# Kernel tuning notes

Measured on AMD Instinct MI355X. Metric: run time of the kernel, lower is better.

## Reference

```python
import jax, jax.numpy as jnp
import numpy as np

H = 2048      # hidden_size
I = 768       # moe_intermediate_size
E = 32        # num_experts
K = 8         # num_experts_per_tok (top_k)
T = 1024      # tokens (batch * seq)


def setup_inputs() -> dict:
    key = jax.random.key(0)
    k1, k2, k3, k4 = jax.random.split(key, 4)
    return {
        "hidden_states": jax.random.normal(k1, (T, H), jnp.float32),
        "gate_weight": jax.random.normal(k2, (E, H), jnp.float32) * 0.02,
        "w13_weight": jax.random.normal(k3, (E, 2 * I, H), jnp.float32) * 0.02,
        "w2_weight": jax.random.normal(k4, (E, H, I), jnp.float32) * 0.02,
    }


def reference(hidden_states, gate_weight, w13_weight, w2_weight):
    x = hidden_states  # [T, H]
    # --- router (Qwen3MoeSparseMoeBlock gating) ---
    logits = x @ gate_weight.T                      # [T, E]
    probs = jax.nn.softmax(logits, axis=-1)
    topk_w, topk_idx = jax.lax.top_k(probs, K)      # [T, K]
    topk_w = topk_w / jnp.sum(topk_w, axis=-1, keepdims=True)  # norm_topk_prob
    # dense combine matrix [T, E]: routing weight per (token, expert), 0 if not selected
    combine = jnp.zeros((x.shape[0], E), x.dtype).at[
        jnp.arange(x.shape[0])[:, None], topk_idx
    ].add(topk_w)
    # --- expert FFNs (fused gate+up = w13, SiLU-gated, then w2 down-proj) ---
    h = jnp.einsum('th,eoh->eto', x, w13_weight)    # [E, T, 2I]
    gate, up = h[:, :, :I], h[:, :, I:]
    act = jax.nn.silu(gate) * up                    # [E, T, I]
    y = jnp.einsum('eti,ehi->eth', act, w2_weight)  # [E, T, H]
    # --- weighted combine ---
    return jnp.einsum('eth,te->th', y, combine)     # [T, H]
```

## Files before the change

### kernel.cpp

```cpp
#include <hip/hip_runtime.h>
#include <hip/hip_bf16.h>
#include <math.h>

#define T_TOK 1024
#define H_DIM 2048
#define I_DIM 768
#define E_NUM 32
#define K_TOP 8
#define BK 32
#define GRID_P 1024

typedef __bf16 bf16x8 __attribute__((ext_vector_type(8)));
typedef float  f32x4  __attribute__((ext_vector_type(4)));

__device__ __forceinline__ bf16x8 cvt2_bf16(const f32x4 a, const f32x4 b) {
    bf16x8 r;
    r[0] = (__bf16)a[0]; r[1] = (__bf16)a[1]; r[2] = (__bf16)a[2]; r[3] = (__bf16)a[3];
    r[4] = (__bf16)b[0]; r[5] = (__bf16)b[1]; r[6] = (__bf16)b[2]; r[7] = (__bf16)b[3];
    return r;
}

__device__ __forceinline__ int frag_off(int r, int kgrp8) {
    return (r >> 4) * 512 + kgrp8 * 128 + (r & 15) * 8;
}

__global__ __launch_bounds__(256) void cvtx_kernel(
    const float* __restrict__ x, __bf16* __restrict__ xb)
{
    const int i = (blockIdx.x * 256 + threadIdx.x) * 8;
    const f32x4 a = *(const f32x4*)(x + i);
    const f32x4 b = *(const f32x4*)(x + i + 4);
    *(bf16x8*)(xb + i) = cvt2_bf16(a, b);
}

__global__ __launch_bounds__(256) void router_kernel(
    const float* __restrict__ x, const float* __restrict__ gw,
    float* __restrict__ wdense, unsigned int* __restrict__ masks)
{
    const int t = blockIdx.x;
    const int tid = threadIdx.x;
    __shared__ float part[256];
    __shared__ float logits[E_NUM];
    const int e = tid & 31;
    const int chunk = tid >> 5;
    const float* xr = x + (size_t)t * H_DIM;
    const float* gr = gw + (size_t)e * H_DIM;
    const int base = chunk * (H_DIM / 8);
    float s = 0.f;
    for (int h = 0; h < H_DIM / 8; h += 4) {
        const f32x4 xv = *reinterpret_cast<const f32x4*>(xr + base + h);
        const f32x4 gv = *reinterpret_cast<const f32x4*>(gr + base + h);
        s += xv[0]*gv[0] + xv[1]*gv[1] + xv[2]*gv[2] + xv[3]*gv[3];
    }
    part[tid] = s;
    __syncthreads();
    if (tid < E_NUM) {
        float tot = 0.f;
        for (int c = 0; c < 8; ++c) tot += part[c * 32 + tid];
        logits[tid] = tot;
    }
    __syncthreads();
    if (tid == 0) {
        float l[E_NUM];
        for (int i = 0; i < E_NUM; ++i) {
            l[i] = logits[i];
            wdense[(size_t)t * E_NUM + i] = 0.f;
        }
        unsigned mask = 0;
        int   idx[K_TOP];
        float lv[K_TOP];
        for (int k = 0; k < K_TOP; ++k) {
            float best = -1e30f; int bi = 0;
            for (int i = 0; i < E_NUM; ++i)
                if (!((mask >> i) & 1u) && l[i] > best) { best = l[i]; bi = i; }
            mask |= (1u << bi); idx[k] = bi; lv[k] = best;
        }
        const float m = lv[0];
        float den = 0.f;
        for (int k = 0; k < K_TOP; ++k) den += expf(lv[k] - m);
        for (int k = 0; k < K_TOP; ++k)
            wdense[(size_t)t * E_NUM + idx[k]] = expf(lv[k] - m) / den;
        masks[t] = mask;
    }
}

__global__ __launch_bounds__(256) void count_kernel(
    const unsigned int* __restrict__ masks, int* __restrict__ cnt)
{
    const int e = blockIdx.x;
    const int tid = threadIdx.x;
    int c = 0;
    for (int t = tid; t < T_TOK; t += 256) c += (masks[t] >> e) & 1u;
    __shared__ int red[256];
    red[tid] = c; __syncthreads();
    for (int s = 128; s > 0; s >>= 1) {
        if (tid < s) red[tid] += red[tid + s];
        __syncthreads();
    }
    if (tid == 0) cnt[e] = red[0];
}

__global__ void scan_kernel(const int* __restrict__ cnt, int* __restrict__ off,
                            int* __restrict__ tbl)
{
    if (threadIdx.x == 0 && blockIdx.x == 0) {
        int r = 0, nt = 0;
        for (int e = 0; e < E_NUM; ++e) {
            off[e] = r;
            const int c = cnt[e];
            r += c;
            const int t = (c + 127) >> 7;
            for (int z = 0; z < t; ++z) tbl[1 + nt++] = (e << 8) | z;
        }
        tbl[0] = nt;
    }
}

__global__ __launch_bounds__(256) void fill_kernel(
    const unsigned int* __restrict__ masks, const float* __restrict__ wdense,
    const int* __restrict__ off, int* __restrict__ tok, float* __restrict__ wgt,
    int* __restrict__ posl)
{
    const int e = blockIdx.x;
    const int tid = threadIdx.x;
    const int PER = T_TOK / 256;
    int sel[PER]; int c = 0;
    for (int i = 0; i < PER; ++i) {
        const int t = tid * PER + i;
        sel[i] = (masks[t] >> e) & 1u;
        c += sel[i];
    }
    __shared__ int s[256];
    s[tid] = c; __syncthreads();
    if (tid == 0) {
        int r = 0;
        for (int j = 0; j < 256; ++j) { int v = s[j]; s[j] = r; r += v; }
    }
    __syncthreads();
    int pos = off[e] + s[tid];
    for (int i = 0; i < PER; ++i) {
        if (sel[i]) {
            const int t = tid * PER + i;
            tok[pos] = t;
            wgt[pos] = wdense[(size_t)t * E_NUM + e];
            const int slot = __popc(masks[t] & ((1u << e) - 1u));
            posl[t * K_TOP + slot] = pos;
            pos++;
        }
    }
}

#define GEMM_PHASE(P, Q)                                                       \
  {                                                                            \
    if (scur + 2 < NS) {                                                       \
      const int kk = (scur + 2) * BK;                                          \
      pa##P##_0 = *(const bf16x8*)(ap + kk);                                   \
      pa##P##_1 = *(const bf16x8*)(ap + kk + 8);                               \
      pb##P##_0 = *(const f32x4*)(wp + kk);                                    \
      pb##P##_1 = *(const f32x4*)(wp + kk + 4);                                \
      pb##P##_2 = *(const f32x4*)(wp + kk + 8);                                \
      pb##P##_3 = *(const f32x4*)(wp + kk + 12);                               \
    }                                                                          \
    bf16x8 af[4], bfr[4];                                                      \
    _Pragma("unroll")                                                          \
    for (int m = 0; m < 4; ++m)                                                \
      af[m] = *(const bf16x8*)&As[P][((wm >> 4) + m) * 512 + lane * 8];        \
    _Pragma("unroll")                                                          \
    for (int n = 0; n < 4; ++n)                                                \
      bfr[n] = *(const bf16x8*)&Bs[P][(wn * 4 + n) * 512 + lane * 8];          \
    _Pragma("unroll")                                                          \
    for (int m = 0; m < 4; ++m)                                                \
      _Pragma("unroll")                                                        \
      for (int n = 0; n < 4; ++n)                                              \
        acc[m][n] = __builtin_amdgcn_mfma_f32_16x16x32_bf16(af[m], bfr[n],     \
                                                            acc[m][n], 0,0,0); \
    if (scur + 1 < NS) {                                                       \
      *(bf16x8*)&As[Q][wo]       = pa##Q##_0;                                  \
      *(bf16x8*)&As[Q][wo + 128] = pa##Q##_1;                                  \
      *(bf16x8*)&Bs[Q][wo]       = cvt2_bf16(pb##Q##_0, pb##Q##_1);            \
      *(bf16x8*)&Bs[Q][wo + 128] = cvt2_bf16(pb##Q##_2, pb##Q##_3);            \
    }                                                                          \
    asm volatile("s_waitcnt lgkmcnt(0)" ::: "memory");                         \
    __builtin_amdgcn_s_barrier();                                              \
    ++scur;                                                                    \
  }

#define GEMM_PROLOGUE()                                                        \
    pa0_0 = *(const bf16x8*)(ap);                                              \
    pa0_1 = *(const bf16x8*)(ap + 8);                                          \
    pb0_0 = *(const f32x4*)(wp);                                               \
    pb0_1 = *(const f32x4*)(wp + 4);                                           \
    pb0_2 = *(const f32x4*)(wp + 8);                                           \
    pb0_3 = *(const f32x4*)(wp + 12);                                          \
    pa1_0 = *(const bf16x8*)(ap + BK);                                         \
    pa1_1 = *(const bf16x8*)(ap + BK + 8);                                     \
    pb1_0 = *(const f32x4*)(wp + BK);                                          \
    pb1_1 = *(const f32x4*)(wp + BK + 4);                                      \
    pb1_2 = *(const f32x4*)(wp + BK + 8);                                      \
    pb1_3 = *(const f32x4*)(wp + BK + 12);                                     \
    *(bf16x8*)&As[0][wo]       = pa0_0;                                        \
    *(bf16x8*)&As[0][wo + 128] = pa0_1;                                        \
    *(bf16x8*)&Bs[0][wo]       = cvt2_bf16(pb0_0, pb0_1);                      \
    *(bf16x8*)&Bs[0][wo + 128] = cvt2_bf16(pb0_2, pb0_3);                      \
    asm volatile("s_waitcnt lgkmcnt(0)" ::: "memory");                         \
    __builtin_amdgcn_s_barrier();

__global__ __launch_bounds__(256, 3) void gemm1_kernel(
    const __bf16* __restrict__ xb, const float* __restrict__ w13,
    const int* __restrict__ tok, const int* __restrict__ cnt,
    const int* __restrict__ off, const int* __restrict__ tbl,
    unsigned short* __restrict__ act)
{
    __shared__ __bf16 As[2][4096];
    __shared__ __bf16 Bs[2][4096];
    const int tid  = threadIdx.x;
    const int wid  = tid >> 6;
    const int lane = tid & 63;
    const int wm = (wid >> 1) * 64;
    const int wn = (wid & 1);
    const int lrow = lane & 15;
    const int sr = tid >> 1;
    const int kh = tid & 1;
    const int wo = frag_off(sr, kh * 2);
    const int NS = H_DIM / BK;

    const int W = tbl[0] * 12;
    for (int w = blockIdx.x; w < W; w += gridDim.x) {
        const int ti   = w / 12;
        const int nidx = w - ti * 12;
        const int ez = tbl[1 + ti];
        const int e  = ez >> 8;
        const int m0 = (ez & 255) * 128;
        const int c  = cnt[e];
        const int o  = off[e];
        const int n0 = nidx * 64;

        int rA = m0 + sr; rA = rA < c ? rA : c - 1;
        const __bf16* ap = xb + (size_t)tok[o + rA] * H_DIM + kh * 16;
        const int grp = sr >> 5;
        const int wrow = (grp & 1) * I_DIM + n0 + (grp >> 1) * 32 + (sr & 31);
        const float* wp = w13 + (size_t)e * (2 * I_DIM) * H_DIM
                              + (size_t)wrow * H_DIM + kh * 16;

        bf16x8 pa0_0, pa0_1, pa1_0, pa1_1;
        f32x4  pb0_0, pb0_1, pb0_2, pb0_3, pb1_0, pb1_1, pb1_2, pb1_3;
        f32x4  acc[4][4] = {};

        GEMM_PROLOGUE()

        int scur = 0;
        for (int it = 0; it < NS; it += 2) {
            GEMM_PHASE(0, 1)
            GEMM_PHASE(1, 0)
        }

#pragma unroll
        for (int m = 0; m < 4; ++m)
#pragma unroll
            for (int n = 0; n < 2; ++n)
#pragma unroll
                for (int i = 0; i < 4; ++i) {
                    const int row = m0 + wm + m * 16 + (lane >> 4) * 4 + i;
                    if (row < c) {
                        const int icol = n0 + wn * 32 + n * 16 + lrow;
                        const float g = acc[m][n][i];
                        const float u = acc[m][n + 2][i];
                        const float a = (g / (1.f + expf(-g))) * u;
                        act[(size_t)(o + row) * I_DIM + icol] =
                            __builtin_bit_cast(unsigned short, (__bf16)a);
                    }
                }
    }
}

__global__ __launch_bounds__(256, 3) void gemm2_kernel(
    const unsigned short* __restrict__ act, const float* __restrict__ w2,
    const int* __restrict__ tok, const float* __restrict__ wgt,
    const int* __restrict__ cnt, const int* __restrict__ off,
    const int* __restrict__ tbl, float* __restrict__ ybuf)
{
    __shared__ __bf16 As[2][4096];
    __shared__ __bf16 Bs[2][4096];
    const int tid  = threadIdx.x;
    const int wid  = tid >> 6;
    const int lane = tid & 63;
    const int wm = (wid >> 1) * 64;
    const int wn = (wid & 1);
    const int lrow = lane & 15;
    const int sr = tid >> 1;
    const int kh = tid & 1;
    const int wo = frag_off(sr, kh * 2);
    const int NS = I_DIM / BK;

    const int W = tbl[0] * 16;
    for (int w = blockIdx.x; w < W; w += gridDim.x) {
        const int ti   = w >> 4;
        const int nidx = w & 15;
        const int ez = tbl[1 + ti];
        const int e  = ez >> 8;
        const int m0 = (ez & 255) * 128;
        const int c  = cnt[e];
        const int o  = off[e];
        const int n0 = nidx * 128;

        int rA = m0 + sr; rA = rA < c ? rA : c - 1;
        const __bf16* ap = (const __bf16*)act + (size_t)(o + rA) * I_DIM + kh * 16;
        const float* wp = w2 + (size_t)e * H_DIM * I_DIM
                             + (size_t)(n0 + sr) * I_DIM + kh * 16;

        bf16x8 pa0_0, pa0_1, pa1_0, pa1_1;
        f32x4  pb0_0, pb0_1, pb0_2, pb0_3, pb1_0, pb1_1, pb1_2, pb1_3;
        f32x4  acc[4][4] = {};

        GEMM_PROLOGUE()

        int scur = 0;
        for (int it = 0; it < NS; it += 2) {
            GEMM_PHASE(0, 1)
            GEMM_PHASE(1, 0)
        }

#pragma unroll
        for (int m = 0; m < 4; ++m)
#pragma unroll
            for (int i = 0; i < 4; ++i) {
                const int row = m0 + wm + m * 16 + (lane >> 4) * 4 + i;
                if (row < c) {
                    const float wv = wgt[o + row];
                    float* yr = ybuf + (size_t)(o + row) * H_DIM + n0 + wn * 64 + lrow;
#pragma unroll
                    for (int n = 0; n < 4; ++n)
                        yr[n * 16] = wv * acc[m][n][i];
                }
            }
    }
}

__global__ __launch_bounds__(256) void combine_kernel(
    const float* __restrict__ ybuf, const int* __restrict__ posl,
    float* __restrict__ out)
{
    const int t = blockIdx.x;
    int p[K_TOP];
#pragma unroll
    for (int s = 0; s < K_TOP; ++s) p[s] = posl[t * K_TOP + s];
    const int h0 = threadIdx.x * 4;
#pragma unroll
    for (int hh = h0; hh < H_DIM; hh += 1024) {
        f32x4 a = {0.f, 0.f, 0.f, 0.f};
#pragma unroll
        for (int s = 0; s < K_TOP; ++s) {
            const f32x4 v = *(const f32x4*)(ybuf + (size_t)p[s] * H_DIM + hh);
            a[0] += v[0]; a[1] += v[1]; a[2] += v[2]; a[3] += v[3];
        }
        *(f32x4*)(out + (size_t)t * H_DIM + hh) = a;
    }
}

extern "C" void kernel_launch(void* const* d_in, const int* in_sizes, int n_in,
                              void* d_out, int out_size, void* d_ws, size_t ws_size,
                              hipStream_t stream)
{
    const float* x   = (const float*)d_in[0];
    const float* gw  = (const float*)d_in[1];
    const float* w13 = (const float*)d_in[2];
    const float* w2  = (const float*)d_in[3];
    float* out = (float*)d_out;

    char* ws = (char*)d_ws;
    float*          wdense = (float*)(ws + 0x00000);
    unsigned int*   masks  = (unsigned int*)(ws + 0x20000);
    int*            cnt    = (int*)(ws + 0x21000);
    int*            off    = (int*)(ws + 0x21800);
    int*            tbl    = (int*)(ws + 0x22000);
    int*            tok    = (int*)(ws + 0x23000);
    float*          wgt    = (float*)(ws + 0x2B000);
    unsigned short* act    = (unsigned short*)(ws + 0x33000);
    __bf16*         xb     = (__bf16*)(ws + 0xC40000);
    int*            posl   = (int*)(ws + 0x1040000);
    float*          ybuf   = (float*)(ws + 0x1100000);

    cvtx_kernel<<<(T_TOK * H_DIM) / (256 * 8), 256, 0, stream>>>(x, xb);
    router_kernel<<<T_TOK, 256, 0, stream>>>(x, gw, wdense, masks);
    count_kernel<<<E_NUM, 256, 0, stream>>>(masks, cnt);
    scan_kernel<<<1, 64, 0, stream>>>(cnt, off, tbl);
    fill_kernel<<<E_NUM, 256, 0, stream>>>(masks, wdense, off, tok, wgt, posl);
    gemm1_kernel<<<GRID_P, 256, 0, stream>>>(xb, w13, tok, cnt, off, tbl, act);
    gemm2_kernel<<<GRID_P, 256, 0, stream>>>(act, w2, tok, wgt, cnt, off, tbl, ybuf);
    combine_kernel<<<T_TOK, 256, 0, stream>>>(ybuf, posl, out);
}
```

Measured before the change: 351.5 us.

## Load A tiles directly to LDS and fuse x conversion into router

The bf16 activation (A) tiles in both expert GEMMs are now fetched with global_load_lds straight into shared memory, replacing the register-staged loads and LDS stores. The waitcnt is split so that only the A tile's vector-memory loads are awaited while the B prefetch stays in flight. The standalone fp32-to-bf16 conversion of x is folded into the router kernel, which removes one launch and one extra pass over x. In exchange, the A-tile LDS layout now depends on the per-lane address mapping matching the MFMA fragment layout, and correctness relies on the hand-set vmcnt counts.

```diff
diff --git a/kernel.cpp b/kernel.cpp
--- a/kernel.cpp
+++ b/kernel.cpp
@@ -24,23 +24,31 @@
     return (r >> 4) * 512 + kgrp8 * 128 + (r & 15) * 8;
 }
 
-__global__ __launch_bounds__(256) void cvtx_kernel(
-    const float* __restrict__ x, __bf16* __restrict__ xb)
-{
-    const int i = (blockIdx.x * 256 + threadIdx.x) * 8;
-    const f32x4 a = *(const f32x4*)(x + i);
-    const f32x4 b = *(const f32x4*)(x + i + 4);
-    *(bf16x8*)(xb + i) = cvt2_bf16(a, b);
+__device__ __forceinline__ void gl_lds16(const void* g, void* l) {
+    typedef const unsigned int __attribute__((address_space(1)))* gp_t;
+    typedef unsigned int __attribute__((address_space(3)))* lp_t;
+    gp_t gp = reinterpret_cast<gp_t>(reinterpret_cast<unsigned long long>(g));
+    lp_t lp = reinterpret_cast<lp_t>((unsigned int)reinterpret_cast<unsigned long long>(l));
+    __builtin_amdgcn_global_load_lds(gp, lp, 16, 0, 0);
 }
 
 __global__ __launch_bounds__(256) void router_kernel(
     const float* __restrict__ x, const float* __restrict__ gw,
-    float* __restrict__ wdense, unsigned int* __restrict__ masks)
+    float* __restrict__ wdense, unsigned int* __restrict__ masks,
+    __bf16* __restrict__ xb)
 {
     const int t = blockIdx.x;
     const int tid = threadIdx.x;
     __shared__ float part[256];
     __shared__ float logits[E_NUM];
+
+    {
+        const float* xr2 = x + (size_t)t * H_DIM + tid * 8;
+        const f32x4 a = *(const f32x4*)(xr2);
+        const f32x4 b = *(const f32x4*)(xr2 + 4);
+        *(bf16x8*)(xb + (size_t)t * H_DIM + tid * 8) = cvt2_bf16(a, b);
+    }
+
     const int e = tid & 31;
     const int chunk = tid >> 5;
     const float* xr = x + (size_t)t * H_DIM;
@@ -152,10 +160,15 @@
 
 #define GEMM_PHASE(P, Q)                                                       \
   {                                                                            \
+    if (scur + 1 < NS) {                                                       \
+      const int k1 = (scur + 1) * BK;                                          \
+      __builtin_amdgcn_sched_barrier(0);                                       \
+      gl_lds16(agp0 + k1, &As[Q][widA]);                                       \
+      gl_lds16(agp1 + k1, &As[Q][widA + 512]);                                 \
+      __builtin_amdgcn_sched_barrier(0);                                       \
+    }                                                                          \
     if (scur + 2 < NS) {                                                       \
       const int kk = (scur + 2) * BK;                                          \
-      pa##P##_0 = *(const bf16x8*)(ap + kk);                                   \
-      pa##P##_1 = *(const bf16x8*)(ap + kk + 8);                               \
       pb##P##_0 = *(const f32x4*)(wp + kk);                                    \
       pb##P##_1 = *(const f32x4*)(wp + kk + 4);                                \
       pb##P##_2 = *(const f32x4*)(wp + kk + 8);                                \
@@ -175,34 +188,33 @@
         acc[m][n] = __builtin_amdgcn_mfma_f32_16x16x32_bf16(af[m], bfr[n],     \
                                                             acc[m][n], 0,0,0); \
     if (scur + 1 < NS) {                                                       \
-      *(bf16x8*)&As[Q][wo]       = pa##Q##_0;                                  \
-      *(bf16x8*)&As[Q][wo + 128] = pa##Q##_1;                                  \
       *(bf16x8*)&Bs[Q][wo]       = cvt2_bf16(pb##Q##_0, pb##Q##_1);            \
       *(bf16x8*)&Bs[Q][wo + 128] = cvt2_bf16(pb##Q##_2, pb##Q##_3);            \
     }                                                                          \
-    asm volatile("s_waitcnt lgkmcnt(0)" ::: "memory");                         \
+    if (scur + 2 < NS)                                                         \
+      asm volatile("s_waitcnt lgkmcnt(0) vmcnt(4)" ::: "memory");              \
+    else                                                                       \
+      asm volatile("s_waitcnt lgkmcnt(0) vmcnt(0)" ::: "memory");              \
     __builtin_amdgcn_s_barrier();                                              \
     ++scur;                                                                    \
   }
 
 #define GEMM_PROLOGUE()                                                        \
-    pa0_0 = *(const bf16x8*)(ap);                                              \
-    pa0_1 = *(const bf16x8*)(ap + 8);                                          \
+    __builtin_amdgcn_sched_barrier(0);                                         \
+    gl_lds16(agp0, &As[0][widA]);                                              \
+    gl_lds16(agp1, &As[0][widA + 512]);                                        \
+    __builtin_amdgcn_sched_barrier(0);                                         \
     pb0_0 = *(const f32x4*)(wp);                                               \
     pb0_1 = *(const f32x4*)(wp + 4);                                           \
     pb0_2 = *(const f32x4*)(wp + 8);                                           \
     pb0_3 = *(const f32x4*)(wp + 12);                                          \
-    pa1_0 = *(const bf16x8*)(ap + BK);                                         \
-    pa1_1 = *(const bf16x8*)(ap + BK + 8);                                     \
     pb1_0 = *(const f32x4*)(wp + BK);                                          \
     pb1_1 = *(const f32x4*)(wp + BK + 4);                                      \
     pb1_2 = *(const f32x4*)(wp + BK + 8);                                      \
     pb1_3 = *(const f32x4*)(wp + BK + 12);                                     \
-    *(bf16x8*)&As[0][wo]       = pa0_0;                                        \
-    *(bf16x8*)&As[0][wo + 128] = pa0_1;                                        \
     *(bf16x8*)&Bs[0][wo]       = cvt2_bf16(pb0_0, pb0_1);                      \
     *(bf16x8*)&Bs[0][wo + 128] = cvt2_bf16(pb0_2, pb0_3);                      \
-    asm volatile("s_waitcnt lgkmcnt(0)" ::: "memory");                         \
+    asm volatile("s_waitcnt lgkmcnt(0) vmcnt(4)" ::: "memory");                \
     __builtin_amdgcn_s_barrier();
 
 __global__ __launch_bounds__(256, 3) void gemm1_kernel(
@@ -211,8 +223,8 @@
     const int* __restrict__ off, const int* __restrict__ tbl,
     unsigned short* __restrict__ act)
 {
-    __shared__ __bf16 As[2][4096];
-    __shared__ __bf16 Bs[2][4096];
+    __shared__ __align__(16) __bf16 As[2][4096];
+    __shared__ __align__(16) __bf16 Bs[2][4096];
     const int tid  = threadIdx.x;
     const int wid  = tid >> 6;
     const int lane = tid & 63;
@@ -222,6 +234,7 @@
     const int sr = tid >> 1;
     const int kh = tid & 1;
     const int wo = frag_off(sr, kh * 2);
+    const int widA = wid * 1024;
     const int NS = H_DIM / BK;
 
     const int W = tbl[0] * 12;
@@ -235,16 +248,21 @@
         const int o  = off[e];
         const int n0 = nidx * 64;
 
-        int rA = m0 + sr; rA = rA < c ? rA : c - 1;
-        const __bf16* ap = xb + (size_t)tok[o + rA] * H_DIM + kh * 16;
+        const __bf16 *agp0, *agp1;
+        {
+            int r0 = m0 + wid * 32 + (lane & 15);      r0 = r0 < c ? r0 : c - 1;
+            int r1 = m0 + wid * 32 + 16 + (lane & 15); r1 = r1 < c ? r1 : c - 1;
+            const int kq = (lane >> 4) * 8;
+            agp0 = xb + (size_t)tok[o + r0] * H_DIM + kq;
+            agp1 = xb + (size_t)tok[o + r1] * H_DIM + kq;
+        }
         const int grp = sr >> 5;
         const int wrow = (grp & 1) * I_DIM + n0 + (grp >> 1) * 32 + (sr & 31);
         const float* wp = w13 + (size_t)e * (2 * I_DIM) * H_DIM
                               + (size_t)wrow * H_DIM + kh * 16;
 
-        bf16x8 pa0_0, pa0_1, pa1_0, pa1_1;
-        f32x4  pb0_0, pb0_1, pb0_2, pb0_3, pb1_0, pb1_1, pb1_2, pb1_3;
-        f32x4  acc[4][4] = {};
+        f32x4 pb0_0, pb0_1, pb0_2, pb0_3, pb1_0, pb1_1, pb1_2, pb1_3;
+        f32x4 acc[4][4] = {};
 
         GEMM_PROLOGUE()
 
@@ -279,8 +297,8 @@
     const int* __restrict__ cnt, const int* __restrict__ off,
     const int* __restrict__ tbl, float* __restrict__ ybuf)
 {
-    __shared__ __bf16 As[2][4096];
-    __shared__ __bf16 Bs[2][4096];
+    __shared__ __align__(16) __bf16 As[2][4096];
+    __shared__ __align__(16) __bf16 Bs[2][4096];
     const int tid  = threadIdx.x;
     const int wid  = tid >> 6;
     const int lane = tid & 63;
@@ -290,6 +308,7 @@
     const int sr = tid >> 1;
     const int kh = tid & 1;
     const int wo = frag_off(sr, kh * 2);
+    const int widA = wid * 1024;
     const int NS = I_DIM / BK;
 
     const int W = tbl[0] * 16;
@@ -303,14 +322,19 @@
         const int o  = off[e];
         const int n0 = nidx * 128;
 
-        int rA = m0 + sr; rA = rA < c ? rA : c - 1;
-        const __bf16* ap = (const __bf16*)act + (size_t)(o + rA) * I_DIM + kh * 16;
+        const __bf16 *agp0, *agp1;
+        {
+            int r0 = m0 + wid * 32 + (lane & 15);      r0 = r0 < c ? r0 : c - 1;
+            int r1 = m0 + wid * 32 + 16 + (lane & 15); r1 = r1 < c ? r1 : c - 1;
+            const int kq = (lane >> 4) * 8;
+            agp0 = (const __bf16*)act + (size_t)(o + r0) * I_DIM + kq;
+            agp1 = (const __bf16*)act + (size_t)(o + r1) * I_DIM + kq;
+        }
         const float* wp = w2 + (size_t)e * H_DIM * I_DIM
                              + (size_t)(n0 + sr) * I_DIM + kh * 16;
 
-        bf16x8 pa0_0, pa0_1, pa1_0, pa1_1;
-        f32x4  pb0_0, pb0_1, pb0_2, pb0_3, pb1_0, pb1_1, pb1_2, pb1_3;
-        f32x4  acc[4][4] = {};
+        f32x4 pb0_0, pb0_1, pb0_2, pb0_3, pb1_0, pb1_1, pb1_2, pb1_3;
+        f32x4 acc[4][4] = {};
 
         GEMM_PROLOGUE()
 
@@ -380,8 +404,7 @@
     int*            posl   = (int*)(ws + 0x1040000);
     float*          ybuf   = (float*)(ws + 0x1100000);
 
-    cvtx_kernel<<<(T_TOK * H_DIM) / (256 * 8), 256, 0, stream>>>(x, xb);
-    router_kernel<<<T_TOK, 256, 0, stream>>>(x, gw, wdense, masks);
+    router_kernel<<<T_TOK, 256, 0, stream>>>(x, gw, wdense, masks, xb);
     count_kernel<<<E_NUM, 256, 0, stream>>>(masks, cnt);
     scan_kernel<<<1, 64, 0, stream>>>(cnt, off, tbl);
     fill_kernel<<<E_NUM, 256, 0, stream>>>(masks, wdense, off, tok, wgt, posl);
```

New measurement: 366.1 us. +4.1%, slower.
